# Performance work log

Hardware: AMD Instinct MI355X
Metric: run time of the kernel (lower is better)

Reference implementation:

```python
import jax, jax.numpy as jnp
import numpy as np

N_NODES = 50000
N_EDGES = 800000
IN_DIM = 128
HIDDEN = 64
HEADS = 4
N_GRAPHS = 256
NEG_SLOPE = 0.2  # PyG GATConv default


def gat_conv(x, src, dst, W, a_src, a_dst, b):
    """PyG-style GATConv (concat=True), eval mode (no dropout).
    x: [N, F_in]; src/dst: [E] (self-loops already included);
    W: [H*C, F_in]; a_src/a_dst: [H, C]; b: [H*C].
    """
    N = x.shape[0]
    H, C = a_src.shape
    h = (x @ W.T).reshape(N, H, C)                      # [N, H, C]
    alo = (h * a_src[None]).sum(-1)                     # [N, H]
    ahi = (h * a_dst[None]).sum(-1)                     # [N, H]
    e = jax.nn.leaky_relu(alo[src] + ahi[dst], NEG_SLOPE)  # [E, H]
    # segment softmax over destination neighborhoods
    m = jax.ops.segment_max(e, dst, num_segments=N)     # [N, H]
    ex = jnp.exp(e - m[dst])
    denom = jax.ops.segment_sum(ex, dst, num_segments=N)
    alpha = ex / (denom[dst] + 1e-16)                   # [E, H]
    out = jax.ops.segment_sum(h[src] * alpha[:, :, None], dst, num_segments=N)
    return out.reshape(N, H * C) + b


def setup_inputs() -> dict:
    key = jax.random.key(0)
    ks = jax.random.split(key, 24)
    p = lambda k, s: (jax.random.normal(k, s, jnp.float32) * 0.1)
    x = jax.random.normal(ks[0], (N_NODES, IN_DIM), jnp.float32)
    edge_index = jax.random.randint(ks[1], (2, N_EDGES), 0, N_NODES, jnp.int64 if jax.config.jax_enable_x64 else jnp.int32)
    batch_idx = jnp.sort(jax.random.randint(ks[2], (N_NODES,), 0, N_GRAPHS))
    HC = HIDDEN * HEADS
    return {
        "x": x, "edge_index": edge_index, "batch_idx": batch_idx,
        "W1": p(ks[3], (HC, IN_DIM)), "as1": p(ks[4], (HEADS, HIDDEN)), "ad1": p(ks[5], (HEADS, HIDDEN)), "b1": jnp.zeros((HC,), jnp.float32),
        "W2": p(ks[6], (HC, HC)), "as2": p(ks[7], (HEADS, HIDDEN)), "ad2": p(ks[8], (HEADS, HIDDEN)), "b2": jnp.zeros((HC,), jnp.float32),
        "W3": p(ks[9], (HIDDEN, HC)), "as3": p(ks[10], (1, HIDDEN)), "ad3": p(ks[11], (1, HIDDEN)), "b3": jnp.zeros((HIDDEN,), jnp.float32),
        "Wc1": p(ks[12], (HIDDEN, HIDDEN)), "bc1": jnp.zeros((HIDDEN,), jnp.float32),
        "Wc2": p(ks[13], (1, HIDDEN)), "bc2": jnp.zeros((1,), jnp.float32),
        "Wr1": p(ks[14], (HIDDEN, HIDDEN)), "br1": jnp.zeros((HIDDEN,), jnp.float32),
        "Wr2": p(ks[15], (1, HIDDEN)), "br2": jnp.zeros((1,), jnp.float32),
    }


def reference(x, edge_index, batch_idx, W1, as1, ad1, b1, W2, as2, ad2, b2, W3, as3, ad3, b3, Wc1, bc1, Wc2, bc2, Wr1, br1, Wr2, br2):
    N = x.shape[0]
    loops = jnp.arange(N, dtype=edge_index.dtype)
    src = jnp.concatenate([edge_index[0], loops])  # add_self_loops=True (PyG default)
    dst = jnp.concatenate([edge_index[1], loops])
    h = jax.nn.elu(gat_conv(x, src, dst, W1, as1, ad1, b1))
    h = jax.nn.elu(gat_conv(h, src, dst, W2, as2, ad2, b2))
    h = jax.nn.elu(gat_conv(h, src, dst, W3, as3, ad3, b3))  # [N, HIDDEN]
    # global mean pool over graphs
    cnt = jax.ops.segment_sum(jnp.ones((N,), h.dtype), batch_idx, num_segments=N_GRAPHS)
    g = jax.ops.segment_sum(h, batch_idx, num_segments=N_GRAPHS) / jnp.maximum(cnt, 1.0)[:, None]
    cls_logit = (jax.nn.relu(g @ Wc1.T + bc1) @ Wc2.T + bc2).reshape(-1)
    reg_pred = (jax.nn.relu(g @ Wr1.T + br1) @ Wr2.T + br2).reshape(-1)
    return (cls_logit, reg_pred)
```

## Files before the change

kernel.cpp:

```cpp
#include <hip/hip_runtime.h>

#define N_NODES 50000
#define N_EDGES 800000
#define EP_EDGES (N_EDGES + N_NODES)
#define N_GRAPHS 256
#define NBLK_SCAN ((N_NODES + 255) / 256)
#define POOL_CHUNK ((N_NODES + 255) / 256)

typedef unsigned short u16;
typedef __attribute__((ext_vector_type(8))) short s8v;
typedef __attribute__((ext_vector_type(4))) float f4v;

__device__ __forceinline__ u16 fb(float f) {
  unsigned u = __float_as_uint(f);
  return (u16)((u + 0x7fffu + ((u >> 16) & 1u)) >> 16);
}
__device__ __forceinline__ float bff(u16 s) {
  return __uint_as_float(((unsigned)s) << 16);
}

__global__ void f2b(const float* __restrict__ in, u16* __restrict__ o, int n) {
  int i = blockIdx.x * 256 + threadIdx.x;
  if (i < n) o[i] = fb(in[i]);
}

__global__ __launch_bounds__(256) void gemm_bf16(
    const u16* __restrict__ A, const u16* __restrict__ W,
    u16* __restrict__ C, int M, int Nout, int K) {
  __shared__ u16 As[64][40];
  __shared__ u16 Bs[64][40];
  const int t = threadIdx.x;
  const int m0 = blockIdx.y * 64, n0 = blockIdx.x * 64;
  const int r = t >> 2, c = t & 3;
  const int w = t >> 6, lane = t & 63;
  const int mi = (w & 1) * 32, ni = (w >> 1) * 32;
  const int quad = lane >> 4, fr = lane & 15;

  f4v c00{}, c01{}, c10{}, c11{};
  for (int k0 = 0; k0 < K; k0 += 32) {
    uint4 av = make_uint4(0, 0, 0, 0);
    int m = m0 + r;
    if (m < M) av = *(const uint4*)&A[(size_t)m * K + k0 + c * 8];
    uint4 bv = *(const uint4*)&W[(size_t)(n0 + r) * K + k0 + c * 8];
    __syncthreads();
    *(uint4*)&As[r][c * 8] = av;
    *(uint4*)&Bs[r][c * 8] = bv;
    __syncthreads();
    s8v a0 = *(const s8v*)&As[mi + fr][quad * 8];
    s8v a1 = *(const s8v*)&As[mi + 16 + fr][quad * 8];
    s8v b0 = *(const s8v*)&Bs[ni + fr][quad * 8];
    s8v b1 = *(const s8v*)&Bs[ni + 16 + fr][quad * 8];
    c00 = __builtin_amdgcn_mfma_f32_16x16x32_bf16(a0, b0, c00, 0, 0, 0);
    c01 = __builtin_amdgcn_mfma_f32_16x16x32_bf16(a0, b1, c01, 0, 0, 0);
    c10 = __builtin_amdgcn_mfma_f32_16x16x32_bf16(a1, b0, c10, 0, 0, 0);
    c11 = __builtin_amdgcn_mfma_f32_16x16x32_bf16(a1, b1, c11, 0, 0, 0);
  }
  const int col = n0 + ni + fr;
#pragma unroll
  for (int i = 0; i < 4; ++i) {
    int row = m0 + mi + quad * 4 + i;
    if (row < M) {
      C[(size_t)row * Nout + col] = fb(c00[i]);
      C[(size_t)row * Nout + col + 16] = fb(c01[i]);
    }
    int row2 = row + 16;
    if (row2 < M) {
      C[(size_t)row2 * Nout + col] = fb(c10[i]);
      C[(size_t)row2 * Nout + col + 16] = fb(c11[i]);
    }
  }
}

__global__ void k_hist(const int* __restrict__ ei, int* __restrict__ deg) {
  int e = blockIdx.x * 256 + threadIdx.x;
  if (e >= EP_EDGES) return;
  int d = (e < N_EDGES) ? ei[N_EDGES + e] : e - N_EDGES;
  atomicAdd(&deg[d], 1);
}

__global__ void k_scan_local(const int* __restrict__ deg,
                             int* __restrict__ rowstart,
                             int* __restrict__ bsum) {
  __shared__ int sh[256];
  const int tid = threadIdx.x;
  const int i = blockIdx.x * 256 + tid;
  int v = (i < N_NODES) ? deg[i] : 0;
  sh[tid] = v;
  __syncthreads();
  for (int off = 1; off < 256; off <<= 1) {
    int add = (tid >= off) ? sh[tid - off] : 0;
    __syncthreads();
    sh[tid] += add;
    __syncthreads();
  }
  if (i < N_NODES) rowstart[i] = sh[tid] - v;
  if (tid == 255) bsum[blockIdx.x] = sh[255];
}

__global__ void k_scan_bsum(int* __restrict__ bsum, int* __restrict__ boff) {
  __shared__ int sh[256];
  const int tid = threadIdx.x;
  int v = (tid < NBLK_SCAN) ? bsum[tid] : 0;
  sh[tid] = v;
  __syncthreads();
  for (int off = 1; off < 256; off <<= 1) {
    int add = (tid >= off) ? sh[tid - off] : 0;
    __syncthreads();
    sh[tid] += add;
    __syncthreads();
  }
  boff[tid] = sh[tid] - v;
}

__global__ void k_scan_add(int* __restrict__ rowstart,
                           const int* __restrict__ boff) {
  int i = blockIdx.x * 256 + threadIdx.x;
  if (i < N_NODES) rowstart[i] += boff[i >> 8];
  if (i == N_NODES) rowstart[N_NODES] = EP_EDGES;
}

__global__ void k_scatter(const int* __restrict__ ei,
                          const int* __restrict__ rowstart,
                          int* __restrict__ fill, int* __restrict__ esrc) {
  int e = blockIdx.x * 256 + threadIdx.x;
  if (e >= EP_EDGES) return;
  int s, d;
  if (e < N_EDGES) { s = ei[e]; d = ei[N_EDGES + e]; }
  else             { s = d = e - N_EDGES; }
  int pos = rowstart[d] + atomicAdd(&fill[d], 1);
  esrc[pos] = s;
}

__global__ void attn_scores(const u16* __restrict__ h,
                            const float* __restrict__ a_src,
                            const float* __restrict__ a_dst,
                            float* __restrict__ alo, float* __restrict__ ahi,
                            int HC, int H) {
  const int n = blockIdx.x;
  const int t = threadIdx.x;
  float v = bff(h[(size_t)n * HC + t]);
  float s = v * a_src[t];
  float d = v * a_dst[t];
#pragma unroll
  for (int off = 32; off; off >>= 1) {
    s += __shfl_down(s, off, 64);
    d += __shfl_down(d, off, 64);
  }
  if ((t & 63) == 0) {
    int hd = t >> 6;
    alo[n * H + hd] = s;
    ahi[n * H + hd] = d;
  }
}

__global__ __launch_bounds__(128) void agg_fused4(
    const int* __restrict__ rowstart, const int* __restrict__ esrc,
    const u16* __restrict__ hbuf, const float* __restrict__ alo,
    const float* __restrict__ ahi, const float* __restrict__ bias,
    u16* __restrict__ feat) {
  const int d = blockIdx.x;
  const int t = threadIdx.x;
  const int c = t * 2;
  const int head = t >> 5;
  const int s0 = rowstart[d], s1 = rowstart[d + 1];
  const float ah = ahi[d * 4 + head];
  float m = -1e30f, l = 0.f, o0 = 0.f, o1 = 0.f;
  for (int i = s0; i < s1; i += 4) {
    float av[4];
    unsigned hv[4];
#pragma unroll
    for (int j = 0; j < 4; ++j) {
      if (i + j < s1) {
        int s = esrc[i + j];
        av[j] = alo[s * 4 + head];
        hv[j] = *(const unsigned*)&hbuf[(size_t)s * 256 + c];
      } else {
        av[j] = -1e38f;
        hv[j] = 0;
      }
    }
#pragma unroll
    for (int j = 0; j < 4; ++j) {
      float e = av[j] + ah;
      e = e > 0.f ? e : 0.2f * e;
      float mn = fmaxf(m, e);
      float sc = __expf(m - mn);
      float w = __expf(e - mn);
      l = l * sc + w;
      o0 = o0 * sc + w * bff((u16)(hv[j] & 0xffffu));
      o1 = o1 * sc + w * bff((u16)(hv[j] >> 16));
      m = mn;
    }
  }
  float inv = 1.f / (l + 1e-16f);
  float v0 = o0 * inv + bias[c], v1 = o1 * inv + bias[c + 1];
  v0 = v0 > 0.f ? v0 : __expf(v0) - 1.f;
  v1 = v1 > 0.f ? v1 : __expf(v1) - 1.f;
  unsigned pv = (unsigned)fb(v0) | ((unsigned)fb(v1) << 16);
  *(unsigned*)&feat[(size_t)d * 256 + c] = pv;
}

__global__ __launch_bounds__(64) void agg_fused1(
    const int* __restrict__ rowstart, const int* __restrict__ esrc,
    const u16* __restrict__ hbuf, const float* __restrict__ alo,
    const float* __restrict__ ahi, const float* __restrict__ bias,
    float* __restrict__ feat) {
  const int d = blockIdx.x;
  const int t = threadIdx.x;
  const int s0 = rowstart[d], s1 = rowstart[d + 1];
  const float ah = ahi[d];
  float m = -1e30f, l = 0.f, o = 0.f;
  for (int i = s0; i < s1; i += 4) {
    float av[4];
    u16 hv[4];
#pragma unroll
    for (int j = 0; j < 4; ++j) {
      if (i + j < s1) {
        int s = esrc[i + j];
        av[j] = alo[s];
        hv[j] = hbuf[(size_t)s * 64 + t];
      } else {
        av[j] = -1e38f;
        hv[j] = 0;
      }
    }
#pragma unroll
    for (int j = 0; j < 4; ++j) {
      float e = av[j] + ah;
      e = e > 0.f ? e : 0.2f * e;
      float mn = fmaxf(m, e);
      float sc = __expf(m - mn);
      float w = __expf(e - mn);
      l = l * sc + w;
      o = o * sc + w * bff(hv[j]);
      m = mn;
    }
  }
  float v = o / (l + 1e-16f) + bias[t];
  feat[(size_t)d * 64 + t] = v > 0.f ? v : __expf(v) - 1.f;
}

__global__ __launch_bounds__(64) void pool_seg(
    const float* __restrict__ feat, const int* __restrict__ batch,
    float* __restrict__ gsum, float* __restrict__ gcnt) {
  const int b = blockIdx.x;
  const int t = threadIdx.x;
  int n0 = b * POOL_CHUNK;
  int n1 = n0 + POOL_CHUNK;
  if (n1 > N_NODES) n1 = N_NODES;
  if (n0 >= n1) return;
  int g = batch[n0];
  float acc = 0.f;
  int cnt = 0;
  for (int n = n0; n < n1; ++n) {
    int gn = batch[n];
    if (gn != g) {
      atomicAdd(&gsum[g * 64 + t], acc);
      if (t == 0) atomicAdd(&gcnt[g], (float)cnt);
      acc = 0.f; cnt = 0; g = gn;
    }
    acc += feat[(size_t)n * 64 + t];
    ++cnt;
  }
  atomicAdd(&gsum[g * 64 + t], acc);
  if (t == 0) atomicAdd(&gcnt[g], (float)cnt);
}

__global__ void heads(const float* __restrict__ gsum,
                      const float* __restrict__ gcnt,
                      const float* __restrict__ Wc1, const float* __restrict__ bc1,
                      const float* __restrict__ Wc2, const float* __restrict__ bc2,
                      const float* __restrict__ Wr1, const float* __restrict__ br1,
                      const float* __restrict__ Wr2, const float* __restrict__ br2,
                      float* __restrict__ out) {
  __shared__ float g[64];
  const int gi = blockIdx.x, j = threadIdx.x;
  float cnt = gcnt[gi];
  cnt = cnt < 1.f ? 1.f : cnt;
  g[j] = gsum[gi * 64 + j] / cnt;
  __syncthreads();
  float hc = bc1[j], hr = br1[j];
#pragma unroll 8
  for (int c = 0; c < 64; ++c) {
    float gv = g[c];
    hc += gv * Wc1[j * 64 + c];
    hr += gv * Wr1[j * 64 + c];
  }
  hc = fmaxf(hc, 0.f) * Wc2[j];
  hr = fmaxf(hr, 0.f) * Wr2[j];
#pragma unroll
  for (int off = 32; off; off >>= 1) {
    hc += __shfl_down(hc, off, 64);
    hr += __shfl_down(hr, off, 64);
  }
  if (j == 0) {
    out[gi] = hc + bc2[0];
    out[N_GRAPHS + gi] = hr + br2[0];
  }
}

extern "C" void kernel_launch(void* const* d_in, const int* in_sizes, int n_in,
                              void* d_out, int out_size, void* d_ws,
                              size_t ws_size, hipStream_t stream) {
  const float* x   = (const float*)d_in[0];
  const int* ei    = (const int*)d_in[1];
  const int* batch = (const int*)d_in[2];
  const float* W1  = (const float*)d_in[3];
  const float* as1 = (const float*)d_in[4];
  const float* ad1 = (const float*)d_in[5];
  const float* b1  = (const float*)d_in[6];
  const float* W2  = (const float*)d_in[7];
  const float* as2 = (const float*)d_in[8];
  const float* ad2 = (const float*)d_in[9];
  const float* b2  = (const float*)d_in[10];
  const float* W3  = (const float*)d_in[11];
  const float* as3 = (const float*)d_in[12];
  const float* ad3 = (const float*)d_in[13];
  const float* b3  = (const float*)d_in[14];
  const float* Wc1 = (const float*)d_in[15];
  const float* bc1 = (const float*)d_in[16];
  const float* Wc2 = (const float*)d_in[17];
  const float* bc2 = (const float*)d_in[18];
  const float* Wr1 = (const float*)d_in[19];
  const float* br1 = (const float*)d_in[20];
  const float* Wr2 = (const float*)d_in[21];
  const float* br2 = (const float*)d_in[22];
  float* out = (float*)d_out;

  float* ws = (float*)d_ws;
  u16* h_buf = (u16*)ws;
  float* p = ws + (size_t)N_NODES * 128;
  u16* featb = (u16*)p;
  p += (size_t)N_NODES * 128;
  u16* xb = (u16*)p;
  p += (size_t)N_NODES * 64;
  u16* W1b = (u16*)p; p += 16384;
  u16* W2b = (u16*)p; p += 32768;
  u16* W3b = (u16*)p; p += 8192;
  float* feat3 = p;   p += (size_t)N_NODES * 64;
  float* alo   = p;   p += (size_t)N_NODES * 4;
  float* ahi   = p;   p += (size_t)N_NODES * 4;
  int* rowstart = (int*)p; p += (N_NODES + 4);
  int* esrc    = (int*)p;  p += EP_EDGES;
  float* gsum  = p;   p += N_GRAPHS * 64;
  float* gcnt  = p;
  int* deg  = (int*)alo;
  int* fill = (int*)ahi;
  int* bsum = (int*)gsum;
  int* boff = (int*)gsum + 256;

  hipMemsetAsync(deg, 0, (size_t)N_NODES * 4, stream);
  hipMemsetAsync(fill, 0, (size_t)N_NODES * 4, stream);
  const int eblk = (EP_EDGES + 255) / 256;
  k_hist<<<eblk, 256, 0, stream>>>(ei, deg);
  k_scan_local<<<NBLK_SCAN, 256, 0, stream>>>(deg, rowstart, bsum);
  k_scan_bsum<<<1, 256, 0, stream>>>(bsum, boff);
  k_scan_add<<<(N_NODES + 256) / 256, 256, 0, stream>>>(rowstart, boff);
  k_scatter<<<eblk, 256, 0, stream>>>(ei, rowstart, fill, esrc);

  f2b<<<(N_NODES * 128 + 255) / 256, 256, 0, stream>>>(x, xb, N_NODES * 128);
  f2b<<<(32768 + 255) / 256, 256, 0, stream>>>(W1, W1b, 32768);
  f2b<<<(65536 + 255) / 256, 256, 0, stream>>>(W2, W2b, 65536);
  f2b<<<(16384 + 255) / 256, 256, 0, stream>>>(W3, W3b, 16384);

  const int MB = (N_NODES + 63) / 64;
  gemm_bf16<<<dim3(4, MB), 256, 0, stream>>>(xb, W1b, h_buf, N_NODES, 256, 128);
  attn_scores<<<N_NODES, 256, 0, stream>>>(h_buf, as1, ad1, alo, ahi, 256, 4);
  agg_fused4<<<N_NODES, 128, 0, stream>>>(rowstart, esrc, h_buf, alo, ahi, b1,
                                          featb);
  gemm_bf16<<<dim3(4, MB), 256, 0, stream>>>(featb, W2b, h_buf, N_NODES, 256, 256);
  attn_scores<<<N_NODES, 256, 0, stream>>>(h_buf, as2, ad2, alo, ahi, 256, 4);
  agg_fused4<<<N_NODES, 128, 0, stream>>>(rowstart, esrc, h_buf, alo, ahi, b2,
                                          featb);
  gemm_bf16<<<dim3(1, MB), 256, 0, stream>>>(featb, W3b, h_buf, N_NODES, 64, 256);
  attn_scores<<<N_NODES, 64, 0, stream>>>(h_buf, as3, ad3, alo, ahi, 64, 1);
  agg_fused1<<<N_NODES, 64, 0, stream>>>(rowstart, esrc, h_buf, alo, ahi, b3,
                                         feat3);

  hipMemsetAsync(gsum, 0, (size_t)N_GRAPHS * 64 * 4, stream);
  hipMemsetAsync(gcnt, 0, (size_t)N_GRAPHS * 4, stream);
  pool_seg<<<N_GRAPHS, 64, 0, stream>>>(feat3, batch, gsum, gcnt);
  heads<<<N_GRAPHS, 64, 0, stream>>>(gsum, gcnt, Wc1, bc1, Wc2, bc2, Wr1, br1,
                                     Wr2, br2, out);
}
```

Before: 595.2 us.

## Replace online softmax with two-pass lane-parallel softmax and staged weighted gather

The GAT aggregation kernels drop the per-edge serial online softmax. They now compute the max and the sum of exponentials in parallel across lanes, with wave shuffle reductions. The normalized edge weights and source indices are staged in shared memory in chunks of 32 or 64 edges, and the feature gather runs 8 edges at a time with plain accumulation and no rescaling. This removes the two exps and the rescale per edge per thread, and lets more gather loads be in flight at once. In exchange it reads esrc and alo three times and adds block barriers per chunk.

```diff
diff --git a/kernel.cpp b/kernel.cpp
--- a/kernel.cpp
+++ b/kernel.cpp
@@ -153,54 +153,84 @@
   }
 }
 
-__global__ __launch_bounds__(128) void agg_fused4(
+__global__ __launch_bounds__(128) void agg2_4(
     const int* __restrict__ rowstart, const int* __restrict__ esrc,
     const u16* __restrict__ hbuf, const float* __restrict__ alo,
     const float* __restrict__ ahi, const float* __restrict__ bias,
     u16* __restrict__ feat) {
   const int d = blockIdx.x;
   const int t = threadIdx.x;
+  const int lane32 = t & 31;
+  const int head = t >> 5;
   const int c = t * 2;
-  const int head = t >> 5;
   const int s0 = rowstart[d], s1 = rowstart[d + 1];
   const float ah = ahi[d * 4 + head];
-  float m = -1e30f, l = 0.f, o0 = 0.f, o1 = 0.f;
-  for (int i = s0; i < s1; i += 4) {
-    float av[4];
-    unsigned hv[4];
-#pragma unroll
-    for (int j = 0; j < 4; ++j) {
-      if (i + j < s1) {
-        int s = esrc[i + j];
-        av[j] = alo[s * 4 + head];
-        hv[j] = *(const unsigned*)&hbuf[(size_t)s * 256 + c];
-      } else {
-        av[j] = -1e38f;
-        hv[j] = 0;
+
+  float mx = -1e30f;
+  for (int j = s0 + lane32; j < s1; j += 32) {
+    int s = esrc[j];
+    float e = alo[s * 4 + head] + ah;
+    e = e > 0.f ? e : 0.2f * e;
+    mx = fmaxf(mx, e);
+  }
+#pragma unroll
+  for (int off = 16; off; off >>= 1) mx = fmaxf(mx, __shfl_xor(mx, off, 64));
+  float sm = 0.f;
+  for (int j = s0 + lane32; j < s1; j += 32) {
+    int s = esrc[j];
+    float e = alo[s * 4 + head] + ah;
+    e = e > 0.f ? e : 0.2f * e;
+    sm += __expf(e - mx);
+  }
+#pragma unroll
+  for (int off = 16; off; off >>= 1) sm += __shfl_xor(sm, off, 64);
+  const float linv = 1.f / (sm + 1e-16f);
+
+  __shared__ float wls[32][4];
+  __shared__ int sld[32];
+  float o0 = 0.f, o1 = 0.f;
+  for (int base = s0; base < s1; base += 32) {
+    int j = base + lane32;
+    int s = d;
+    float w = 0.f;
+    if (j < s1) {
+      s = esrc[j];
+      float e = alo[s * 4 + head] + ah;
+      e = e > 0.f ? e : 0.2f * e;
+      w = __expf(e - mx) * linv;
+    }
+    __syncthreads();
+    wls[lane32][head] = w;
+    if (t < 32) sld[lane32] = s;
+    __syncthreads();
+    int cnt8 = (min(32, s1 - base) + 7) & ~7;
+    for (int jj = 0; jj < cnt8; jj += 8) {
+      float w2[8];
+      int ss[8];
+      unsigned hv[8];
+#pragma unroll
+      for (int q = 0; q < 8; ++q) {
+        ss[q] = sld[jj + q];
+        w2[q] = wls[jj + q][head];
       }
-    }
-#pragma unroll
-    for (int j = 0; j < 4; ++j) {
-      float e = av[j] + ah;
-      e = e > 0.f ? e : 0.2f * e;
-      float mn = fmaxf(m, e);
-      float sc = __expf(m - mn);
-      float w = __expf(e - mn);
-      l = l * sc + w;
-      o0 = o0 * sc + w * bff((u16)(hv[j] & 0xffffu));
-      o1 = o1 * sc + w * bff((u16)(hv[j] >> 16));
-      m = mn;
-    }
-  }
-  float inv = 1.f / (l + 1e-16f);
-  float v0 = o0 * inv + bias[c], v1 = o1 * inv + bias[c + 1];
+#pragma unroll
+      for (int q = 0; q < 8; ++q)
+        hv[q] = *(const unsigned*)&hbuf[(size_t)ss[q] * 256 + c];
+#pragma unroll
+      for (int q = 0; q < 8; ++q) {
+        o0 += w2[q] * bff((u16)(hv[q] & 0xffffu));
+        o1 += w2[q] * bff((u16)(hv[q] >> 16));
+      }
+    }
+  }
+  float v0 = o0 + bias[c], v1 = o1 + bias[c + 1];
   v0 = v0 > 0.f ? v0 : __expf(v0) - 1.f;
   v1 = v1 > 0.f ? v1 : __expf(v1) - 1.f;
   unsigned pv = (unsigned)fb(v0) | ((unsigned)fb(v1) << 16);
   *(unsigned*)&feat[(size_t)d * 256 + c] = pv;
 }
 
-__global__ __launch_bounds__(64) void agg_fused1(
+__global__ __launch_bounds__(64) void agg2_1(
     const int* __restrict__ rowstart, const int* __restrict__ esrc,
     const u16* __restrict__ hbuf, const float* __restrict__ alo,
     const float* __restrict__ ahi, const float* __restrict__ bias,
@@ -209,34 +239,61 @@
   const int t = threadIdx.x;
   const int s0 = rowstart[d], s1 = rowstart[d + 1];
   const float ah = ahi[d];
-  float m = -1e30f, l = 0.f, o = 0.f;
-  for (int i = s0; i < s1; i += 4) {
-    float av[4];
-    u16 hv[4];
-#pragma unroll
-    for (int j = 0; j < 4; ++j) {
-      if (i + j < s1) {
-        int s = esrc[i + j];
-        av[j] = alo[s];
-        hv[j] = hbuf[(size_t)s * 64 + t];
-      } else {
-        av[j] = -1e38f;
-        hv[j] = 0;
+
+  float mx = -1e30f;
+  for (int j = s0 + t; j < s1; j += 64) {
+    int s = esrc[j];
+    float e = alo[s] + ah;
+    e = e > 0.f ? e : 0.2f * e;
+    mx = fmaxf(mx, e);
+  }
+#pragma unroll
+  for (int off = 32; off; off >>= 1) mx = fmaxf(mx, __shfl_xor(mx, off, 64));
+  float sm = 0.f;
+  for (int j = s0 + t; j < s1; j += 64) {
+    int s = esrc[j];
+    float e = alo[s] + ah;
+    e = e > 0.f ? e : 0.2f * e;
+    sm += __expf(e - mx);
+  }
+#pragma unroll
+  for (int off = 32; off; off >>= 1) sm += __shfl_xor(sm, off, 64);
+  const float linv = 1.f / (sm + 1e-16f);
+
+  __shared__ float wls[64];
+  __shared__ int sld[64];
+  float o = 0.f;
+  for (int base = s0; base < s1; base += 64) {
+    int j = base + t;
+    int s = d;
+    float w = 0.f;
+    if (j < s1) {
+      s = esrc[j];
+      float e = alo[s] + ah;
+      e = e > 0.f ? e : 0.2f * e;
+      w = __expf(e - mx) * linv;
+    }
+    __syncthreads();
+    wls[t] = w;
+    sld[t] = s;
+    __syncthreads();
+    int cnt8 = (min(64, s1 - base) + 7) & ~7;
+    for (int jj = 0; jj < cnt8; jj += 8) {
+      float w2[8];
+      int ss[8];
+      u16 hv[8];
+#pragma unroll
+      for (int q = 0; q < 8; ++q) {
+        ss[q] = sld[jj + q];
+        w2[q] = wls[jj + q];
       }
-    }
-#pragma unroll
-    for (int j = 0; j < 4; ++j) {
-      float e = av[j] + ah;
-      e = e > 0.f ? e : 0.2f * e;
-      float mn = fmaxf(m, e);
-      float sc = __expf(m - mn);
-      float w = __expf(e - mn);
-      l = l * sc + w;
-      o = o * sc + w * bff(hv[j]);
-      m = mn;
-    }
-  }
-  float v = o / (l + 1e-16f) + bias[t];
+#pragma unroll
+      for (int q = 0; q < 8; ++q) hv[q] = hbuf[(size_t)ss[q] * 64 + t];
+#pragma unroll
+      for (int q = 0; q < 8; ++q) o += w2[q] * bff(hv[q]);
+    }
+  }
+  float v = o + bias[t];
   feat[(size_t)d * 64 + t] = v > 0.f ? v : __expf(v) - 1.f;
 }
 
@@ -366,16 +423,16 @@
   const int MB = (N_NODES + 63) / 64;
   gemm_bf16<<<dim3(4, MB), 256, 0, stream>>>(xb, W1b, h_buf, N_NODES, 256, 128);
   attn_scores<<<N_NODES, 256, 0, stream>>>(h_buf, as1, ad1, alo, ahi, 256, 4);
-  agg_fused4<<<N_NODES, 128, 0, stream>>>(rowstart, esrc, h_buf, alo, ahi, b1,
-                                          featb);
+  agg2_4<<<N_NODES, 128, 0, stream>>>(rowstart, esrc, h_buf, alo, ahi, b1,
+                                      featb);
   gemm_bf16<<<dim3(4, MB), 256, 0, stream>>>(featb, W2b, h_buf, N_NODES, 256, 256);
   attn_scores<<<N_NODES, 256, 0, stream>>>(h_buf, as2, ad2, alo, ahi, 256, 4);
-  agg_fused4<<<N_NODES, 128, 0, stream>>>(rowstart, esrc, h_buf, alo, ahi, b2,
-                                          featb);
+  agg2_4<<<N_NODES, 128, 0, stream>>>(rowstart, esrc, h_buf, alo, ahi, b2,
+                                      featb);
   gemm_bf16<<<dim3(1, MB), 256, 0, stream>>>(featb, W3b, h_buf, N_NODES, 64, 256);
   attn_scores<<<N_NODES, 64, 0, stream>>>(h_buf, as3, ad3, alo, ahi, 64, 1);
-  agg_fused1<<<N_NODES, 64, 0, stream>>>(rowstart, esrc, h_buf, alo, ahi, b3,
-                                         feat3);
+  agg2_1<<<N_NODES, 64, 0, stream>>>(rowstart, esrc, h_buf, alo, ahi, b3,
+                                     feat3);
 
   hipMemsetAsync(gsum, 0, (size_t)N_GRAPHS * 64 * 4, stream);
   hipMemsetAsync(gcnt, 0, (size_t)N_GRAPHS * 4, stream);
```

New measurement: 569.2 us. -4.4%, faster.

## Replace online softmax with two-pass unnormalized softmax in GAT aggregation

Applied to the files above, without the earlier changes.

The aggregation kernels now compute the softmax denominator in a first parallel pass over the neighbor list, then accumulate normalized weights without a running max or rescaling. This drops the serial max/rescale chain and one exp per edge. The 4-head kernel also moves to one 64-lane wave with 4 features per lane and 8-byte loads. Separately, the four f32-to-bf16 conversions become one launch and adjacent memsets are merged. Skipping max subtraction risks overflow if attention logits were large.

```diff
diff --git a/kernel.cpp b/kernel.cpp
--- a/kernel.cpp
+++ b/kernel.cpp
@@ -15,13 +15,29 @@
   unsigned u = __float_as_uint(f);
   return (u16)((u + 0x7fffu + ((u >> 16) & 1u)) >> 16);
 }
+__device__ __forceinline__ float bfl(unsigned p) {
+  return __uint_as_float(p << 16);
+}
+__device__ __forceinline__ float bfh(unsigned p) {
+  return __uint_as_float(p & 0xffff0000u);
+}
 __device__ __forceinline__ float bff(u16 s) {
   return __uint_as_float(((unsigned)s) << 16);
 }
 
-__global__ void f2b(const float* __restrict__ in, u16* __restrict__ o, int n) {
+#define F2B_N0 (N_NODES * 128)
+#define F2B_N1 (F2B_N0 + 32768)
+#define F2B_N2 (F2B_N1 + 65536)
+#define F2B_N3 (F2B_N2 + 16384)
+__global__ void f2b4(const float* __restrict__ x, const float* __restrict__ w1,
+                     const float* __restrict__ w2, const float* __restrict__ w3,
+                     u16* __restrict__ xb, u16* __restrict__ w1b,
+                     u16* __restrict__ w2b, u16* __restrict__ w3b) {
   int i = blockIdx.x * 256 + threadIdx.x;
-  if (i < n) o[i] = fb(in[i]);
+  if (i < F2B_N0) xb[i] = fb(x[i]);
+  else if (i < F2B_N1) w1b[i - F2B_N0] = fb(w1[i - F2B_N0]);
+  else if (i < F2B_N2) w2b[i - F2B_N1] = fb(w2[i - F2B_N1]);
+  else if (i < F2B_N3) w3b[i - F2B_N2] = fb(w3[i - F2B_N2]);
 }
 
 __global__ __launch_bounds__(256) void gemm_bf16(
@@ -153,54 +169,71 @@
   }
 }
 
-__global__ __launch_bounds__(128) void agg_fused4(
+__global__ __launch_bounds__(64) void agg3_4(
     const int* __restrict__ rowstart, const int* __restrict__ esrc,
     const u16* __restrict__ hbuf, const float* __restrict__ alo,
     const float* __restrict__ ahi, const float* __restrict__ bias,
     u16* __restrict__ feat) {
   const int d = blockIdx.x;
-  const int t = threadIdx.x;
-  const int c = t * 2;
-  const int head = t >> 5;
+  const int lane = threadIdx.x;
+  const int head = lane >> 4;
+  const int l16 = lane & 15;
+  const int c = lane * 4;
   const int s0 = rowstart[d], s1 = rowstart[d + 1];
   const float ah = ahi[d * 4 + head];
-  float m = -1e30f, l = 0.f, o0 = 0.f, o1 = 0.f;
-  for (int i = s0; i < s1; i += 4) {
-    float av[4];
-    unsigned hv[4];
-#pragma unroll
-    for (int j = 0; j < 4; ++j) {
-      if (i + j < s1) {
-        int s = esrc[i + j];
-        av[j] = alo[s * 4 + head];
-        hv[j] = *(const unsigned*)&hbuf[(size_t)s * 256 + c];
-      } else {
-        av[j] = -1e38f;
-        hv[j] = 0;
-      }
-    }
-#pragma unroll
-    for (int j = 0; j < 4; ++j) {
-      float e = av[j] + ah;
+
+  float sm = 0.f;
+  for (int j = s0 + l16; j < s1; j += 16) {
+    int s = esrc[j];
+    float e = alo[s * 4 + head] + ah;
+    e = e > 0.f ? e : 0.2f * e;
+    sm += __expf(e);
+  }
+#pragma unroll
+  for (int off = 8; off; off >>= 1) sm += __shfl_xor(sm, off, 64);
+  const float linv = 1.f / (sm + 1e-16f);
+
+  float o0 = 0.f, o1 = 0.f, o2 = 0.f, o3 = 0.f;
+  for (int j = s0; j < s1; j += 4) {
+    int ss[4];
+    float wq[4];
+#pragma unroll
+    for (int q = 0; q < 4; ++q) {
+      int jj = j + q;
+      int sv = esrc[jj < EP_EDGES ? jj : EP_EDGES - 1];
+      ss[q] = (jj < s1) ? sv : d;
+    }
+#pragma unroll
+    for (int q = 0; q < 4; ++q) {
+      float e = alo[ss[q] * 4 + head] + ah;
       e = e > 0.f ? e : 0.2f * e;
-      float mn = fmaxf(m, e);
-      float sc = __expf(m - mn);
-      float w = __expf(e - mn);
-      l = l * sc + w;
-      o0 = o0 * sc + w * bff((u16)(hv[j] & 0xffffu));
-      o1 = o1 * sc + w * bff((u16)(hv[j] >> 16));
-      m = mn;
-    }
-  }
-  float inv = 1.f / (l + 1e-16f);
-  float v0 = o0 * inv + bias[c], v1 = o1 * inv + bias[c + 1];
+      wq[q] = (j + q < s1) ? __expf(e) * linv : 0.f;
+    }
+    uint2 hv[4];
+#pragma unroll
+    for (int q = 0; q < 4; ++q)
+      hv[q] = *(const uint2*)&hbuf[(size_t)ss[q] * 256 + c];
+#pragma unroll
+    for (int q = 0; q < 4; ++q) {
+      o0 += wq[q] * bfl(hv[q].x);
+      o1 += wq[q] * bfh(hv[q].x);
+      o2 += wq[q] * bfl(hv[q].y);
+      o3 += wq[q] * bfh(hv[q].y);
+    }
+  }
+  float4 bv = *(const float4*)&bias[c];
+  float v0 = o0 + bv.x, v1 = o1 + bv.y, v2 = o2 + bv.z, v3 = o3 + bv.w;
   v0 = v0 > 0.f ? v0 : __expf(v0) - 1.f;
   v1 = v1 > 0.f ? v1 : __expf(v1) - 1.f;
-  unsigned pv = (unsigned)fb(v0) | ((unsigned)fb(v1) << 16);
-  *(unsigned*)&feat[(size_t)d * 256 + c] = pv;
-}
-
-__global__ __launch_bounds__(64) void agg_fused1(
+  v2 = v2 > 0.f ? v2 : __expf(v2) - 1.f;
+  v3 = v3 > 0.f ? v3 : __expf(v3) - 1.f;
+  uint2 pv;
+  pv.x = (unsigned)fb(v0) | ((unsigned)fb(v1) << 16);
+  pv.y = (unsigned)fb(v2) | ((unsigned)fb(v3) << 16);
+  *(uint2*)&feat[(size_t)d * 256 + c] = pv;
+}
+
+__global__ __launch_bounds__(64) void agg3_1(
     const int* __restrict__ rowstart, const int* __restrict__ esrc,
     const u16* __restrict__ hbuf, const float* __restrict__ alo,
     const float* __restrict__ ahi, const float* __restrict__ bias,
@@ -209,34 +242,41 @@
   const int t = threadIdx.x;
   const int s0 = rowstart[d], s1 = rowstart[d + 1];
   const float ah = ahi[d];
-  float m = -1e30f, l = 0.f, o = 0.f;
-  for (int i = s0; i < s1; i += 4) {
-    float av[4];
+
+  float sm = 0.f;
+  for (int j = s0 + t; j < s1; j += 64) {
+    int s = esrc[j];
+    float e = alo[s] + ah;
+    e = e > 0.f ? e : 0.2f * e;
+    sm += __expf(e);
+  }
+#pragma unroll
+  for (int off = 32; off; off >>= 1) sm += __shfl_xor(sm, off, 64);
+  const float linv = 1.f / (sm + 1e-16f);
+
+  float o = 0.f;
+  for (int j = s0; j < s1; j += 4) {
+    int ss[4];
+    float wq[4];
+#pragma unroll
+    for (int q = 0; q < 4; ++q) {
+      int jj = j + q;
+      int sv = esrc[jj < EP_EDGES ? jj : EP_EDGES - 1];
+      ss[q] = (jj < s1) ? sv : d;
+    }
+#pragma unroll
+    for (int q = 0; q < 4; ++q) {
+      float e = alo[ss[q]] + ah;
+      e = e > 0.f ? e : 0.2f * e;
+      wq[q] = (j + q < s1) ? __expf(e) * linv : 0.f;
+    }
     u16 hv[4];
 #pragma unroll
-    for (int j = 0; j < 4; ++j) {
-      if (i + j < s1) {
-        int s = esrc[i + j];
-        av[j] = alo[s];
-        hv[j] = hbuf[(size_t)s * 64 + t];
-      } else {
-        av[j] = -1e38f;
-        hv[j] = 0;
-      }
-    }
-#pragma unroll
-    for (int j = 0; j < 4; ++j) {
-      float e = av[j] + ah;
-      e = e > 0.f ? e : 0.2f * e;
-      float mn = fmaxf(m, e);
-      float sc = __expf(m - mn);
-      float w = __expf(e - mn);
-      l = l * sc + w;
-      o = o * sc + w * bff(hv[j]);
-      m = mn;
-    }
-  }
-  float v = o / (l + 1e-16f) + bias[t];
+    for (int q = 0; q < 4; ++q) hv[q] = hbuf[(size_t)ss[q] * 64 + t];
+#pragma unroll
+    for (int q = 0; q < 4; ++q) o += wq[q] * bff(hv[q]);
+  }
+  float v = o + bias[t];
   feat[(size_t)d * 64 + t] = v > 0.f ? v : __expf(v) - 1.f;
 }
 
@@ -345,12 +385,11 @@
   float* gsum  = p;   p += N_GRAPHS * 64;
   float* gcnt  = p;
   int* deg  = (int*)alo;
-  int* fill = (int*)ahi;
+  int* fill = (int*)alo + N_NODES;
   int* bsum = (int*)gsum;
   int* boff = (int*)gsum + 256;
 
-  hipMemsetAsync(deg, 0, (size_t)N_NODES * 4, stream);
-  hipMemsetAsync(fill, 0, (size_t)N_NODES * 4, stream);
+  hipMemsetAsync(deg, 0, (size_t)2 * N_NODES * 4, stream);
   const int eblk = (EP_EDGES + 255) / 256;
   k_hist<<<eblk, 256, 0, stream>>>(ei, deg);
   k_scan_local<<<NBLK_SCAN, 256, 0, stream>>>(deg, rowstart, bsum);
@@ -358,27 +397,24 @@
   k_scan_add<<<(N_NODES + 256) / 256, 256, 0, stream>>>(rowstart, boff);
   k_scatter<<<eblk, 256, 0, stream>>>(ei, rowstart, fill, esrc);
 
-  f2b<<<(N_NODES * 128 + 255) / 256, 256, 0, stream>>>(x, xb, N_NODES * 128);
-  f2b<<<(32768 + 255) / 256, 256, 0, stream>>>(W1, W1b, 32768);
-  f2b<<<(65536 + 255) / 256, 256, 0, stream>>>(W2, W2b, 65536);
-  f2b<<<(16384 + 255) / 256, 256, 0, stream>>>(W3, W3b, 16384);
+  f2b4<<<(F2B_N3 + 255) / 256, 256, 0, stream>>>(x, W1, W2, W3, xb, W1b, W2b,
+                                                 W3b);
 
   const int MB = (N_NODES + 63) / 64;
   gemm_bf16<<<dim3(4, MB), 256, 0, stream>>>(xb, W1b, h_buf, N_NODES, 256, 128);
   attn_scores<<<N_NODES, 256, 0, stream>>>(h_buf, as1, ad1, alo, ahi, 256, 4);
-  agg_fused4<<<N_NODES, 128, 0, stream>>>(rowstart, esrc, h_buf, alo, ahi, b1,
-                                          featb);
+  agg3_4<<<N_NODES, 64, 0, stream>>>(rowstart, esrc, h_buf, alo, ahi, b1,
+                                     featb);
   gemm_bf16<<<dim3(4, MB), 256, 0, stream>>>(featb, W2b, h_buf, N_NODES, 256, 256);
   attn_scores<<<N_NODES, 256, 0, stream>>>(h_buf, as2, ad2, alo, ahi, 256, 4);
-  agg_fused4<<<N_NODES, 128, 0, stream>>>(rowstart, esrc, h_buf, alo, ahi, b2,
-                                          featb);
+  agg3_4<<<N_NODES, 64, 0, stream>>>(rowstart, esrc, h_buf, alo, ahi, b2,
+                                     featb);
   gemm_bf16<<<dim3(1, MB), 256, 0, stream>>>(featb, W3b, h_buf, N_NODES, 64, 256);
   attn_scores<<<N_NODES, 64, 0, stream>>>(h_buf, as3, ad3, alo, ahi, 64, 1);
-  agg_fused1<<<N_NODES, 64, 0, stream>>>(rowstart, esrc, h_buf, alo, ahi, b3,
-                                         feat3);
-
-  hipMemsetAsync(gsum, 0, (size_t)N_GRAPHS * 64 * 4, stream);
-  hipMemsetAsync(gcnt, 0, (size_t)N_GRAPHS * 4, stream);
+  agg3_1<<<N_NODES, 64, 0, stream>>>(rowstart, esrc, h_buf, alo, ahi, b3,
+                                     feat3);
+
+  hipMemsetAsync(gsum, 0, (size_t)(N_GRAPHS * 64 + N_GRAPHS) * 4, stream);
   pool_seg<<<N_GRAPHS, 64, 0, stream>>>(feat3, batch, gsum, gcnt);
   heads<<<N_GRAPHS, 64, 0, stream>>>(gsum, gcnt, Wc1, bc1, Wc2, bc2, Wr1, br1,
                                      Wr2, br2, out);
```

Result: faster. 578.9 us (-2.7%).
